# Optimization experiments

Measured on AMD Instinct MI355X. Metric: run time of the kernel, lower is better.

Reference implementation:

```python
import jax, jax.numpy as jnp
import numpy as np

NEG_INF = -1e30  # finite stand-in for log(0); keeps grads NaN-free

T_, B_, V_, L_ = 1024, 64, 512, 256


def setup_inputs() -> dict:
    key = jax.random.key(0)
    k1, k2 = jax.random.split(key)
    acts = jax.random.normal(k1, (T_, B_, V_), dtype=jnp.float32)
    labels = jax.random.randint(k2, (B_ * L_,), 1, V_, dtype=jnp.int32)  # blank=0 excluded
    act_lens = jnp.full((B_,), T_, dtype=jnp.int32)
    label_lens = jnp.full((B_,), L_, dtype=jnp.int32)
    return {"acts": acts, "labels": labels, "act_lens": act_lens, "label_lens": label_lens}


def _ctc_total_loss(acts, labels, act_lens, label_lens):
    # acts: (T, B, V) raw logits; warp-ctc applies softmax internally.
    T, B, V = acts.shape
    L = labels.shape[0] // B          # static max label length (uniform lengths)
    S = 2 * L + 1                     # extended label lattice with interleaved blanks
    logp = jax.nn.log_softmax(acts, axis=-1)

    # Unflatten labels -> padded (B, L)
    offsets = jnp.concatenate([jnp.zeros((1,), jnp.int32),
                               jnp.cumsum(label_lens.astype(jnp.int32))])[:-1]
    j = jnp.arange(L, dtype=jnp.int32)
    gidx = jnp.clip(offsets[:, None] + j[None, :], 0, labels.shape[0] - 1)
    padded = jnp.where(j[None, :] < label_lens[:, None], labels[gidx], 0)  # (B, L)

    # Extended labels: blank, l1, blank, l2, ..., blank
    ext = jnp.zeros((B, S), dtype=labels.dtype).at[:, 1::2].set(padded)
    ext_m2 = jnp.pad(ext, ((0, 0), (2, 0)))[:, :S]
    allow_skip = (ext != 0) & (ext != ext_m2)
    allow_skip = allow_skip.at[:, :2].set(False)

    bidx = jnp.arange(B)[:, None]
    lp_ext = logp[:, bidx, ext]       # (T, B, S): per-frame log-prob of lattice states

    alpha0 = jnp.full((B, S), NEG_INF, dtype=acts.dtype)
    alpha0 = alpha0.at[:, 0].set(lp_ext[0, :, 0]).at[:, 1].set(lp_ext[0, :, 1])
    neg = jnp.full((B, 1), NEG_INF, dtype=acts.dtype)

    def step(alpha, inp):
        lp_t, t = inp
        a1 = alpha
        a2 = jnp.concatenate([neg, alpha[:, :-1]], axis=1)
        a3 = jnp.concatenate([neg, neg, alpha[:, :-2]], axis=1)
        a3 = jnp.where(allow_skip, a3, NEG_INF)
        new = lp_t + jnp.logaddexp(jnp.logaddexp(a1, a2), a3)
        alpha = jnp.where((t < act_lens)[:, None], new, alpha)  # freeze past act_len
        return alpha, None

    alpha, _ = jax.lax.scan(step, alpha0, (lp_ext[1:], jnp.arange(1, T)))

    s_end = (2 * label_lens).astype(jnp.int32)           # final blank state
    a_end = jnp.take_along_axis(alpha, s_end[:, None], axis=1)[:, 0]
    a_end2 = jnp.take_along_axis(alpha, jnp.maximum(s_end - 1, 0)[:, None], axis=1)[:, 0]
    losses = -jnp.logaddexp(a_end, a_end2)               # per-example NLL
    return jnp.sum(losses)[None]                         # shape (1,), matches FloatTensor([sum])


def reference(acts, labels, act_lens, label_lens):
    return _ctc_total_loss(acts, labels, act_lens, label_lens)
```

## Files before the change

### kernel.cpp

```cpp
#include <hip/hip_runtime.h>

constexpr int T = 1024;
constexpr int B = 64;
constexpr int V = 512;
constexpr int L = 256;
constexpr int S = 2 * L + 1;
constexpr int C = 16;

typedef float f32x4 __attribute__((ext_vector_type(4)));

__device__ __forceinline__ unsigned short f2bf(float f) {
    unsigned u = __float_as_uint(f);
    u += 0x7fffu + ((u >> 16) & 1u);
    return (unsigned short)(u >> 16);
}

__device__ __forceinline__ float lane_bcast(float v, int i) {
    return __uint_as_float((unsigned)__builtin_amdgcn_readlane((int)__float_as_uint(v), i));
}


__global__ __launch_bounds__(64) void offsets_kernel(
    const int* __restrict__ label_lens, int* __restrict__ offsets)
{
    int lane = threadIdx.x;
    int v = (lane < B) ? label_lens[lane] : 0;
    int x = v;
#pragma unroll
    for (int o = 1; o < 64; o <<= 1) {
        int y = __shfl_up(x, o, 64);
        if (lane >= o) x += y;
    }
    if (lane < B) offsets[lane] = x - v;
}

__global__ __launch_bounds__(256) void setup_kernel(
    const float* __restrict__ acts, const int* __restrict__ labels,
    const int* __restrict__ label_lens, const int* __restrict__ offsets,
    float* __restrict__ lse_rows, unsigned short* __restrict__ packedU,
    float* __restrict__ blankU)
{
    __shared__ float rows[4][2][V];
    const int w    = threadIdx.x >> 6;
    const int lane = threadIdx.x & 63;
    const int rbase = (blockIdx.x * 4 + w) * 2;
    const f32x4* p = (const f32x4*)(acts + (size_t)rbase * V);

    f32x4 xa0 = __builtin_nontemporal_load(p + lane);
    f32x4 xa1 = __builtin_nontemporal_load(p + lane + 64);
    f32x4 xb0 = __builtin_nontemporal_load(p + lane + 128);
    f32x4 xb1 = __builtin_nontemporal_load(p + lane + 192);
    f32x4 ea0, ea1, eb0, eb1;
    ea0.x=__expf(xa0.x); ea0.y=__expf(xa0.y); ea0.z=__expf(xa0.z); ea0.w=__expf(xa0.w);
    ea1.x=__expf(xa1.x); ea1.y=__expf(xa1.y); ea1.z=__expf(xa1.z); ea1.w=__expf(xa1.w);
    eb0.x=__expf(xb0.x); eb0.y=__expf(xb0.y); eb0.z=__expf(xb0.z); eb0.w=__expf(xb0.w);
    eb1.x=__expf(xb1.x); eb1.y=__expf(xb1.y); eb1.z=__expf(xb1.z); eb1.w=__expf(xb1.w);
    ((f32x4*)rows[w][0])[lane]      = ea0;
    ((f32x4*)rows[w][0])[lane + 64] = ea1;
    ((f32x4*)rows[w][1])[lane]      = eb0;
    ((f32x4*)rows[w][1])[lane + 64] = eb1;
    float sa = ea0.x+ea0.y+ea0.z+ea0.w + ea1.x+ea1.y+ea1.z+ea1.w;
    float sb = eb0.x+eb0.y+eb0.z+eb0.w + eb1.x+eb1.y+eb1.z+eb1.w;
#pragma unroll
    for (int o = 32; o; o >>= 1) { sa += __shfl_xor(sa, o, 64); sb += __shfl_xor(sb, o, 64); }

#pragma unroll
    for (int rr = 0; rr < 2; ++rr) {
        const int r = rbase + rr;
        const int b = r & (B - 1), t = r >> 6;
        const float* rw = rows[w][rr];
        const int lab_len = label_lens[b];
        const int off     = offsets[b];
        const float ubk   = rw[0];
        const int j0 = 4 * lane;
        float q0 = (j0 + 0 < lab_len) ? rw[labels[min(off + j0 + 0, B * L - 1)]] : ubk;
        float q1 = (j0 + 1 < lab_len) ? rw[labels[min(off + j0 + 1, B * L - 1)]] : ubk;
        float q2 = (j0 + 2 < lab_len) ? rw[labels[min(off + j0 + 2, B * L - 1)]] : ubk;
        float q3 = (j0 + 3 < lab_len) ? rw[labels[min(off + j0 + 3, B * L - 1)]] : ubk;
        ushort4 hv = {f2bf(q0), f2bf(q1), f2bf(q2), f2bf(q3)};
        ((ushort4*)packedU)[(size_t)(b * T + t) * 64 + lane] = hv;
        if (lane == 0) {
            lse_rows[b * T + t] = __logf(rr ? sb : sa);
            blankU[b * T + t]   = ubk;
        }
    }
}

__global__ __launch_bounds__(128, 1) void ctc_kernel(
    const int* __restrict__ labels, const int* __restrict__ act_lens,
    const int* __restrict__ label_lens, const int* __restrict__ offsets,
    const float* __restrict__ lse_rows, const unsigned short* __restrict__ packedU,
    const float* __restrict__ blankU, float* __restrict__ out)
{
    __shared__ float sbr[S];
    __shared__ float s_accb;

    const int b    = blockIdx.x;
    const int wave = threadIdx.x >> 6;
    const int lane = threadIdx.x & 63;
    const int lab_len = label_lens[b];
    const int a_len   = act_lens[b];
    const int th      = (a_len - 1) >> 1;
    const int off     = offsets[b];
    const size_t rowbase = (size_t)b * T;

    int li0 = 4 * lane;
    int eprev = (li0 - 1 >= 0 && li0 - 1 < lab_len) ? labels[min(off + li0 - 1, B * L - 1)] : 0;
    int enext = (li0 + 4 < lab_len) ? labels[min(off + li0 + 4, B * L - 1)] : 0;
    int e0 = (li0 + 0 < lab_len) ? labels[min(off + li0 + 0, B * L - 1)] : 0;
    int e1 = (li0 + 1 < lab_len) ? labels[min(off + li0 + 1, B * L - 1)] : 0;
    int e2 = (li0 + 2 < lab_len) ? labels[min(off + li0 + 2, B * L - 1)] : 0;
    int e3 = (li0 + 3 < lab_len) ? labels[min(off + li0 + 3, B * L - 1)] : 0;

    const float aF0 = (8 * lane + 1 >= 2 && e0 != 0 && e0 != eprev) ? 1.f : 0.f;
    const float aF1 = (e1 != 0 && e1 != e0) ? 1.f : 0.f;
    const float aF2 = (e2 != 0 && e2 != e1) ? 1.f : 0.f;
    const float aF3 = (e3 != 0 && e3 != e2) ? 1.f : 0.f;
    const float aB0 = aF1, aB1 = aF2, aB2 = aF3;
    const float aB3 = (enext != 0 && enext != e3) ? 1.f : 0.f;

    float A0 = 0.f, A1 = 0.f, A2 = 0.f, A3 = 0.f, A4 = 0.f,
          A5 = 0.f, A6 = 0.f, A7 = 0.f, A8 = 0.f;
    float acc = 0.f, sls = 0.f;

    uint2 Ua[C], Ub[C];
    float Ka = 0.f, Kb = 0.f;

#define LOADCH(U, K, TLO) do {                                                \
        const int tl_ = min(max((int)(TLO), 0), T - C);                       \
        const uint2* gp_ = (const uint2*)(packedU + (rowbase + tl_) * 256);   \
        _Pragma("unroll")                                                     \
        for (int i_ = 0; i_ < C; ++i_) U[i_] = gp_[i_ * 64 + lane];           \
        K = blankU[rowbase + tl_ + (lane & (C - 1))];                         \
    } while (0)

#define RESCALE() do {                                                        \
        float m_ = fmaxf(A8, A0); m_ = fmaxf(m_, A1); m_ = fmaxf(m_, A2);     \
        m_ = fmaxf(m_, A3); m_ = fmaxf(m_, A4); m_ = fmaxf(m_, A5);           \
        m_ = fmaxf(m_, A6); m_ = fmaxf(m_, A7);                               \
        _Pragma("unroll")                                                     \
        for (int o_ = 32; o_; o_ >>= 1) m_ = fmaxf(m_, __shfl_xor(m_, o_, 64)); \
        m_ = fmaxf(m_, 1e-30f);                                               \
        float inv_ = __builtin_amdgcn_rcpf(m_);                               \
        acc += __logf(m_);                                                    \
        A0 *= inv_; A1 *= inv_; A2 *= inv_; A3 *= inv_; A4 *= inv_;           \
        A5 *= inv_; A6 *= inv_; A7 *= inv_; A8 *= inv_;                       \
    } while (0)

#define STEPF_CORE(HX, HY, UB) do {                                           \
        const float ub_ = (UB);                                               \
        const unsigned hx_ = (HX), hy_ = (HY);                                \
        const float u0_ = __uint_as_float(hx_ << 16);                         \
        const float u1_ = __uint_as_float(hx_ & 0xffff0000u);                 \
        const float u2_ = __uint_as_float(hy_ << 16);                         \
        const float u3_ = __uint_as_float(hy_ & 0xffff0000u);                 \
        float pA7_ = __shfl_up(A7, 1, 64);                                    \
        if (lane == 0) pA7_ = 0.f;                                            \
        A8 = ub_ * (A8 + A7);                                                 \
        A7 = u3_ * fmaf(aF3, A5, A7 + A6);                                    \
        A6 = ub_ * (A6 + A5);                                                 \
        A5 = u2_ * fmaf(aF2, A3, A5 + A4);                                    \
        A4 = ub_ * (A4 + A3);                                                 \
        A3 = u1_ * fmaf(aF1, A1, A3 + A2);                                    \
        A2 = ub_ * (A2 + A1);                                                 \
        A1 = u0_ * fmaf(aF0, pA7_, A1 + A0);                                  \
        A0 = ub_ * (A0 + pA7_);                                               \
    } while (0)
#define STEPF_R(U, K, I) STEPF_CORE(U[I].x, U[I].y, lane_bcast(K, I))

#define STEPB_CORE(HX, HY, UB) do {                                           \
        const float ub_ = (UB);                                               \
        const unsigned hx_ = (HX), hy_ = (HY);                                \
        const float u0_ = __uint_as_float(hx_ << 16);                         \
        const float u1_ = __uint_as_float(hx_ & 0xffff0000u);                 \
        const float u2_ = __uint_as_float(hy_ << 16);                         \
        const float u3_ = __uint_as_float(hy_ & 0xffff0000u);                 \
        float nC0_ = __shfl_down(A0, 1, 64);                                  \
        if (lane == 63) nC0_ = 0.f;                                           \
        A8 = ub_ * (A8 + A0);                                                 \
        A0 = u0_ * fmaf(aB0, A2, A0 + A1);                                    \
        A1 = ub_ * (A1 + A2);                                                 \
        A2 = u1_ * fmaf(aB1, A4, A2 + A3);                                    \
        A3 = ub_ * (A3 + A4);                                                 \
        A4 = u2_ * fmaf(aB2, A6, A4 + A5);                                    \
        A5 = ub_ * (A5 + A6);                                                 \
        A6 = u3_ * fmaf(aB3, nC0_, A6 + A7);                                  \
        A7 = ub_ * (A7 + nC0_);                                               \
    } while (0)
#define STEPB_R(U, K, I) STEPB_CORE(U[I].x, U[I].y, lane_bcast(K, I))

#define STEP_DIRECT(WHICH, TT) do {                                           \
        uint2 hvd_ = ((const uint2*)(packedU + (rowbase + (TT)) * 256))[lane];\
        float ubd_ = blankU[rowbase + (TT)];                                  \
        WHICH(hvd_.x, hvd_.y, ubd_);                                          \
    } while (0)

    if (wave == 0) {
        for (int t = lane; t < a_len; t += 64) sls += lse_rows[rowbase + t];
#pragma unroll
        for (int o = 32; o; o >>= 1) sls += __shfl_xor(sls, o, 64);

        if (lane == 0) {
            A0 = blankU[rowbase];
            A1 = __uint_as_float(((unsigned)packedU[rowbase * 256]) << 16);
        }

        if (th >= 1) {
            const int kfull = (th - 15) >> 4;
            LOADCH(Ua, Ka, 0);
            LOADCH(Ub, Kb, 16);
#pragma unroll
            for (int i = 1; i < C; ++i) { if (i <= th) STEPF_R(Ua, Ka, i); }
            RESCALE();
            LOADCH(Ua, Ka, 32);
            int k = 1;
            for (; k + 1 <= kfull; k += 2) {
#pragma unroll
                for (int i = 0; i < C; ++i) STEPF_R(Ub, Kb, i);
                RESCALE();
                LOADCH(Ub, Kb, 16 * (k + 2));
#pragma unroll
                for (int i = 0; i < C; ++i) STEPF_R(Ua, Ka, i);
                RESCALE();
                LOADCH(Ua, Ka, 16 * (k + 3));
            }
            if (k <= kfull) {
#pragma unroll
                for (int i = 0; i < C; ++i) STEPF_R(Ub, Kb, i);
                RESCALE();
            }
            const int tS = (kfull >= 1) ? 16 * (kfull + 1) : 16;
            for (int t = tS; t <= th; ++t) {
                STEP_DIRECT(STEPF_CORE, t);
                if (((t - tS) & 7) == 7) RESCALE();
            }
        }
    } else {
        const int send = 2 * lab_len;
        {
            size_t rl = rowbase + (a_len - 1);
            float ubl = blankU[rl];
            float ue  = (lab_len > 0)
                      ? __uint_as_float(((unsigned)packedU[rl * 256 + (lab_len - 1)]) << 16)
                      : 0.f;
            int s0 = 8 * lane + 1;
            A0 = (s0 + 0 == send) ? ubl : ((s0 + 0 == send - 1) ? ue : 0.f);
            A1 = (s0 + 1 == send) ? ubl : ((s0 + 1 == send - 1) ? ue : 0.f);
            A2 = (s0 + 2 == send) ? ubl : ((s0 + 2 == send - 1) ? ue : 0.f);
            A3 = (s0 + 3 == send) ? ubl : ((s0 + 3 == send - 1) ? ue : 0.f);
            A4 = (s0 + 4 == send) ? ubl : ((s0 + 4 == send - 1) ? ue : 0.f);
            A5 = (s0 + 5 == send) ? ubl : ((s0 + 5 == send - 1) ? ue : 0.f);
            A6 = (s0 + 6 == send) ? ubl : ((s0 + 6 == send - 1) ? ue : 0.f);
            A7 = (s0 + 7 == send) ? ubl : ((s0 + 7 == send - 1) ? ue : 0.f);
            A8 = (send == 0) ? ubl : 0.f;
        }

        const int nstB = a_len - 2 - th;
        if (nstB > 0 && a_len >= 16) {
            const int cfull = (a_len - th - 17) >> 4;
            LOADCH(Ua, Ka, a_len - 16);
            LOADCH(Ub, Kb, a_len - 32);
#pragma unroll
            for (int i = C - 2; i >= 0; --i) {
                if (a_len - 16 + i >= th + 1) STEPB_R(Ua, Ka, i);
            }
            RESCALE();
            LOADCH(Ua, Ka, a_len - 48);
            int c = 1;
            for (; c + 1 <= cfull; c += 2) {
#pragma unroll
                for (int i = C - 1; i >= 0; --i) STEPB_R(Ub, Kb, i);
                RESCALE();
                LOADCH(Ub, Kb, a_len - 16 * (c + 3));
#pragma unroll
                for (int i = C - 1; i >= 0; --i) STEPB_R(Ua, Ka, i);
                RESCALE();
                LOADCH(Ua, Ka, a_len - 16 * (c + 4));
            }
            if (c <= cfull) {
#pragma unroll
                for (int i = C - 1; i >= 0; --i) STEPB_R(Ub, Kb, i);
                RESCALE();
            }
            const int cf = (cfull >= 1) ? cfull : 0;
            const int tE = a_len - 16 * (cf + 1) - 1;
            for (int t = tE; t >= th + 1; --t) {
                STEP_DIRECT(STEPB_CORE, t);
                if (((tE - t) & 7) == 7) RESCALE();
            }
        } else if (nstB > 0) {
            for (int t = a_len - 2; t >= th + 1; --t) {
                STEP_DIRECT(STEPB_CORE, t);
                if (((a_len - 2 - t) & 7) == 7) RESCALE();
            }
        }

        {
            float nC0 = __shfl_down(A0, 1, 64);
            if (lane == 63) nC0 = 0.f;
            float w1 = fmaf(aB0, A2, A0 + A1);
            float w2 = A1 + A2;
            float w3 = fmaf(aB1, A4, A2 + A3);
            float w4 = A3 + A4;
            float w5 = fmaf(aB2, A6, A4 + A5);
            float w6 = A5 + A6;
            float w7 = fmaf(aB3, nC0, A6 + A7);
            float w8 = A7 + nC0;
            int sB = 8 * lane + 1;
            sbr[sB + 0] = w1; sbr[sB + 1] = w2; sbr[sB + 2] = w3; sbr[sB + 3] = w4;
            sbr[sB + 4] = w5; sbr[sB + 5] = w6; sbr[sB + 6] = w7; sbr[sB + 7] = w8;
            if (lane == 0) sbr[0] = A8 + A0;
            if (lane == 0) s_accb = acc;
        }
    }
    __syncthreads();
    if (wave == 0) {
        int s0 = 8 * lane;
        float p0 = __logf(fmaxf(A0, 1e-37f)) + __logf(fmaxf(sbr[s0 + 0], 1e-37f));
        float p1 = __logf(fmaxf(A1, 1e-37f)) + __logf(fmaxf(sbr[s0 + 1], 1e-37f));
        float p2 = __logf(fmaxf(A2, 1e-37f)) + __logf(fmaxf(sbr[s0 + 2], 1e-37f));
        float p3 = __logf(fmaxf(A3, 1e-37f)) + __logf(fmaxf(sbr[s0 + 3], 1e-37f));
        float p4 = __logf(fmaxf(A4, 1e-37f)) + __logf(fmaxf(sbr[s0 + 4], 1e-37f));
        float p5 = __logf(fmaxf(A5, 1e-37f)) + __logf(fmaxf(sbr[s0 + 5], 1e-37f));
        float p6 = __logf(fmaxf(A6, 1e-37f)) + __logf(fmaxf(sbr[s0 + 6], 1e-37f));
        float p7 = __logf(fmaxf(A7, 1e-37f)) + __logf(fmaxf(sbr[s0 + 7], 1e-37f));
        float p8 = -3.0e38f;
        if (lane == 63) p8 = __logf(fmaxf(A8, 1e-37f)) + __logf(fmaxf(sbr[512], 1e-37f));
        float pmax = fmaxf(fmaxf(fmaxf(p0, p1), fmaxf(p2, p3)),
                           fmaxf(fmaxf(p4, p5), fmaxf(p6, p7)));
        pmax = fmaxf(pmax, p8);
#pragma unroll
        for (int o = 32; o; o >>= 1) pmax = fmaxf(pmax, __shfl_xor(pmax, o, 64));
        float dot = __expf(p0 - pmax) + __expf(p1 - pmax) + __expf(p2 - pmax)
                  + __expf(p3 - pmax) + __expf(p4 - pmax) + __expf(p5 - pmax)
                  + __expf(p6 - pmax) + __expf(p7 - pmax);
        if (lane == 63) dot += __expf(p8 - pmax);
#pragma unroll
        for (int o = 32; o; o >>= 1) dot += __shfl_xor(dot, o, 64);
        if (lane == 0) {
            float loss = sls - acc - s_accb - (pmax + __logf(dot));
            atomicAdd(out, loss);
        }
    }
#undef LOADCH
#undef RESCALE
#undef STEPF_CORE
#undef STEPF_R
#undef STEPB_CORE
#undef STEPB_R
#undef STEP_DIRECT
}

extern "C" void kernel_launch(void* const* d_in, const int* in_sizes, int n_in,
                              void* d_out, int out_size, void* d_ws, size_t ws_size,
                              hipStream_t stream) {
    const float* acts       = (const float*)d_in[0];
    const int*   labels     = (const int*)d_in[1];
    const int*   act_lens   = (const int*)d_in[2];
    const int*   label_lens = (const int*)d_in[3];
    float*       out        = (float*)d_out;

    float*          lse_rows = (float*)d_ws;
    float*          blankU   = (float*)((char*)d_ws + (size_t)T * B * 4);
    int*            offsets  = (int*)  ((char*)d_ws + (size_t)2 * T * B * 4);
    unsigned short* packedU  = (unsigned short*)((char*)d_ws + (1u << 20));

    hipMemsetAsync(d_out, 0, sizeof(float), stream);

    offsets_kernel<<<1, 64, 0, stream>>>(label_lens, offsets);
    setup_kernel<<<T * B / 8, 256, 0, stream>>>(
        acts, labels, label_lens, offsets, lse_rows, packedU, blankU);
    ctc_kernel<<<B, 128, 0, stream>>>(
        labels, act_lens, label_lens, offsets, lse_rows, packedU, blankU, out);
}
```

Before: 250.4 us.

## Use DPP lane shifts and reductions, triple-buffer chunk loads in CTC recurrence

Replaces the ds_bpermute-based shfl_up/shfl_down neighbour exchange in each recurrence step with DPP wave_shr/wave_shl row moves, and the rescale max-reduction with a DPP row/bcast sequence followed by readlane. Chunk prefetch moves from two register buffers to three, aligned to the step range so the scalar tail loop is removed. Rescaling happens every 8 steps inside the chunk, and the label log-sum-exp reduction is moved after the initial loads are issued. The goal is lower per-step latency on the serial critical path and better hiding of global load latency, at the cost of more registers and DPP semantics that must hold across the whole 64-lane wave.

Measured after the change: 246.3 us. Within noise of the previous version (-1.6%).

```diff
diff --git a/kernel.cpp b/kernel.cpp
--- a/kernel.cpp
+++ b/kernel.cpp
@@ -17,6 +17,21 @@
 
 __device__ __forceinline__ float lane_bcast(float v, int i) {
     return __uint_as_float((unsigned)__builtin_amdgcn_readlane((int)__float_as_uint(v), i));
+}
+
+__device__ __forceinline__ float dpp_shr1z(float x) {
+    return __uint_as_float((unsigned)__builtin_amdgcn_update_dpp(
+        0, (int)__float_as_uint(x), 0x138, 0xf, 0xf, true));
+}
+__device__ __forceinline__ float dpp_shl1z(float x) {
+    return __uint_as_float((unsigned)__builtin_amdgcn_update_dpp(
+        0, (int)__float_as_uint(x), 0x130, 0xf, 0xf, true));
+}
+template <int CTRL, int RM>
+__device__ __forceinline__ float dppmax(float m) {
+    int mi = (int)__float_as_uint(m);
+    int t = __builtin_amdgcn_update_dpp(mi, mi, CTRL, RM, 0xf, false);
+    return fmaxf(m, __uint_as_float((unsigned)t));
 }
 
 
@@ -101,6 +116,7 @@
     const int lab_len = label_lens[b];
     const int a_len   = act_lens[b];
     const int th      = (a_len - 1) >> 1;
+    const int thp1    = th + 1;
     const int off     = offsets[b];
     const size_t rowbase = (size_t)b * T;
 
@@ -123,8 +139,8 @@
           A5 = 0.f, A6 = 0.f, A7 = 0.f, A8 = 0.f;
     float acc = 0.f, sls = 0.f;
 
-    uint2 Ua[C], Ub[C];
-    float Ka = 0.f, Kb = 0.f;
+    uint2 U0[C], U1[C], U2[C];
+    float K0 = 0.f, K1 = 0.f, K2 = 0.f;
 
 #define LOADCH(U, K, TLO) do {                                                \
         const int tl_ = min(max((int)(TLO), 0), T - C);                       \
@@ -138,8 +154,13 @@
         float m_ = fmaxf(A8, A0); m_ = fmaxf(m_, A1); m_ = fmaxf(m_, A2);     \
         m_ = fmaxf(m_, A3); m_ = fmaxf(m_, A4); m_ = fmaxf(m_, A5);           \
         m_ = fmaxf(m_, A6); m_ = fmaxf(m_, A7);                               \
-        _Pragma("unroll")                                                     \
-        for (int o_ = 32; o_; o_ >>= 1) m_ = fmaxf(m_, __shfl_xor(m_, o_, 64)); \
+        m_ = dppmax<0x111, 0xf>(m_);                           \
+        m_ = dppmax<0x112, 0xf>(m_);                           \
+        m_ = dppmax<0x114, 0xf>(m_);                           \
+        m_ = dppmax<0x118, 0xf>(m_);                           \
+        m_ = dppmax<0x142, 0xa>(m_);                 \
+        m_ = dppmax<0x143, 0xc>(m_);                 \
+        m_ = lane_bcast(m_, 63);                                              \
         m_ = fmaxf(m_, 1e-30f);                                               \
         float inv_ = __builtin_amdgcn_rcpf(m_);                               \
         acc += __logf(m_);                                                    \
@@ -154,8 +175,7 @@
         const float u1_ = __uint_as_float(hx_ & 0xffff0000u);                 \
         const float u2_ = __uint_as_float(hy_ << 16);                         \
         const float u3_ = __uint_as_float(hy_ & 0xffff0000u);                 \
-        float pA7_ = __shfl_up(A7, 1, 64);                                    \
-        if (lane == 0) pA7_ = 0.f;                                            \
+        const float pA7_ = dpp_shr1z(A7);                                     \
         A8 = ub_ * (A8 + A7);                                                 \
         A7 = u3_ * fmaf(aF3, A5, A7 + A6);                                    \
         A6 = ub_ * (A6 + A5);                                                 \
@@ -175,8 +195,7 @@
         const float u1_ = __uint_as_float(hx_ & 0xffff0000u);                 \
         const float u2_ = __uint_as_float(hy_ << 16);                         \
         const float u3_ = __uint_as_float(hy_ & 0xffff0000u);                 \
-        float nC0_ = __shfl_down(A0, 1, 64);                                  \
-        if (lane == 63) nC0_ = 0.f;                                           \
+        const float nC0_ = dpp_shl1z(A0);                                     \
         A8 = ub_ * (A8 + A0);                                                 \
         A0 = u0_ * fmaf(aB0, A2, A0 + A1);                                    \
         A1 = ub_ * (A1 + A2);                                                 \
@@ -195,45 +214,73 @@
         WHICH(hvd_.x, hvd_.y, ubd_);                                          \
     } while (0)
 
+#define DOF16(U, K) do {                                                      \
+        _Pragma("unroll")                                                     \
+        for (int i_ = 0; i_ < C; ++i_) {                                      \
+            STEPF_R(U, K, i_);                                                \
+            if (i_ == 7 || i_ == 15) RESCALE();                               \
+        }                                                                     \
+    } while (0)
+#define DOFPART(U, K, TLO) do {                                               \
+        _Pragma("unroll")                                                     \
+        for (int i_ = 0; i_ < C; ++i_) {                                      \
+            if ((TLO) + i_ <= th) STEPF_R(U, K, i_);                          \
+            if (i_ == 7 || i_ == 15) RESCALE();                               \
+        }                                                                     \
+    } while (0)
+#define DOB16(U, K) do {                                                      \
+        _Pragma("unroll")                                                     \
+        for (int i_ = C - 1; i_ >= 0; --i_) {                                 \
+            STEPB_R(U, K, i_);                                                \
+            if (i_ == 8 || i_ == 0) RESCALE();                                \
+        }                                                                     \
+    } while (0)
+#define DOBPART(U, K, TLO) do {                                               \
+        _Pragma("unroll")                                                     \
+        for (int i_ = C - 1; i_ >= 0; --i_) {                                 \
+            if ((TLO) + i_ >= thp1) STEPB_R(U, K, i_);                        \
+            if (i_ == 8 || i_ == 0) RESCALE();                                \
+        }                                                                     \
+    } while (0)
+
     if (wave == 0) {
-        for (int t = lane; t < a_len; t += 64) sls += lse_rows[rowbase + t];
-#pragma unroll
-        for (int o = 32; o; o >>= 1) sls += __shfl_xor(sls, o, 64);
-
         if (lane == 0) {
             A0 = blankU[rowbase];
             A1 = __uint_as_float(((unsigned)packedU[rowbase * 256]) << 16);
         }
 
         if (th >= 1) {
-            const int kfull = (th - 15) >> 4;
-            LOADCH(Ua, Ka, 0);
-            LOADCH(Ub, Kb, 16);
-#pragma unroll
-            for (int i = 1; i < C; ++i) { if (i <= th) STEPF_R(Ua, Ka, i); }
-            RESCALE();
-            LOADCH(Ua, Ka, 32);
-            int k = 1;
-            for (; k + 1 <= kfull; k += 2) {
-#pragma unroll
-                for (int i = 0; i < C; ++i) STEPF_R(Ub, Kb, i);
-                RESCALE();
-                LOADCH(Ub, Kb, 16 * (k + 2));
-#pragma unroll
-                for (int i = 0; i < C; ++i) STEPF_R(Ua, Ka, i);
-                RESCALE();
-                LOADCH(Ua, Ka, 16 * (k + 3));
+            const int nst   = th;
+            const int nc    = (nst + C - 1) / C;
+            const int nfull = nst / C;
+            LOADCH(U0, K0, 1);
+            LOADCH(U1, K1, 1 + C);
+            LOADCH(U2, K2, 1 + 2 * C);
+
+            for (int t = lane; t < a_len; t += 64) sls += lse_rows[rowbase + t];
+#pragma unroll
+            for (int o = 32; o; o >>= 1) sls += __shfl_xor(sls, o, 64);
+
+            int c = 0;
+            for (; c + 3 <= nfull; c += 3) {
+                DOF16(U0, K0); LOADCH(U0, K0, 1 + C * (c + 3));
+                DOF16(U1, K1); LOADCH(U1, K1, 1 + C * (c + 4));
+                DOF16(U2, K2); LOADCH(U2, K2, 1 + C * (c + 5));
             }
-            if (k <= kfull) {
-#pragma unroll
-                for (int i = 0; i < C; ++i) STEPF_R(Ub, Kb, i);
-                RESCALE();
+            const int rem = nfull - c;
+            if (rem == 0) {
+                if (nc > nfull) DOFPART(U0, K0, 1 + C * c);
+            } else if (rem == 1) {
+                DOF16(U0, K0);
+                if (nc > nfull) DOFPART(U1, K1, 1 + C * (c + 1));
+            } else {
+                DOF16(U0, K0); DOF16(U1, K1);
+                if (nc > nfull) DOFPART(U2, K2, 1 + C * (c + 2));
             }
-            const int tS = (kfull >= 1) ? 16 * (kfull + 1) : 16;
-            for (int t = tS; t <= th; ++t) {
-                STEP_DIRECT(STEPF_CORE, t);
-                if (((t - tS) & 7) == 7) RESCALE();
-            }
+        } else {
+            for (int t = lane; t < a_len; t += 64) sls += lse_rows[rowbase + t];
+#pragma unroll
+            for (int o = 32; o; o >>= 1) sls += __shfl_xor(sls, o, 64);
         }
     } else {
         const int send = 2 * lab_len;
@@ -256,48 +303,37 @@
         }
 
         const int nstB = a_len - 2 - th;
-        if (nstB > 0 && a_len >= 16) {
-            const int cfull = (a_len - th - 17) >> 4;
-            LOADCH(Ua, Ka, a_len - 16);
-            LOADCH(Ub, Kb, a_len - 32);
-#pragma unroll
-            for (int i = C - 2; i >= 0; --i) {
-                if (a_len - 16 + i >= th + 1) STEPB_R(Ua, Ka, i);
+        if (nstB > 0 && a_len >= 17) {
+            const int nc    = (nstB + C - 1) / C;
+            const int nfull = nstB / C;
+            LOADCH(U0, K0, a_len - 17);
+            LOADCH(U1, K1, a_len - 17 - C);
+            LOADCH(U2, K2, a_len - 17 - 2 * C);
+            int c = 0;
+            for (; c + 3 <= nfull; c += 3) {
+                DOB16(U0, K0); LOADCH(U0, K0, a_len - 17 - C * (c + 3));
+                DOB16(U1, K1); LOADCH(U1, K1, a_len - 17 - C * (c + 4));
+                DOB16(U2, K2); LOADCH(U2, K2, a_len - 17 - C * (c + 5));
             }
-            RESCALE();
-            LOADCH(Ua, Ka, a_len - 48);
-            int c = 1;
-            for (; c + 1 <= cfull; c += 2) {
-#pragma unroll
-                for (int i = C - 1; i >= 0; --i) STEPB_R(Ub, Kb, i);
-                RESCALE();
-                LOADCH(Ub, Kb, a_len - 16 * (c + 3));
-#pragma unroll
-                for (int i = C - 1; i >= 0; --i) STEPB_R(Ua, Ka, i);
-                RESCALE();
-                LOADCH(Ua, Ka, a_len - 16 * (c + 4));
-            }
-            if (c <= cfull) {
-#pragma unroll
-                for (int i = C - 1; i >= 0; --i) STEPB_R(Ub, Kb, i);
-                RESCALE();
-            }
-            const int cf = (cfull >= 1) ? cfull : 0;
-            const int tE = a_len - 16 * (cf + 1) - 1;
-            for (int t = tE; t >= th + 1; --t) {
-                STEP_DIRECT(STEPB_CORE, t);
-                if (((tE - t) & 7) == 7) RESCALE();
+            const int rem = nfull - c;
+            if (rem == 0) {
+                if (nc > nfull) DOBPART(U0, K0, a_len - 17 - C * c);
+            } else if (rem == 1) {
+                DOB16(U0, K0);
+                if (nc > nfull) DOBPART(U1, K1, a_len - 17 - C * (c + 1));
+            } else {
+                DOB16(U0, K0); DOB16(U1, K1);
+                if (nc > nfull) DOBPART(U2, K2, a_len - 17 - C * (c + 2));
             }
         } else if (nstB > 0) {
-            for (int t = a_len - 2; t >= th + 1; --t) {
+            for (int t = a_len - 2; t >= thp1; --t) {
                 STEP_DIRECT(STEPB_CORE, t);
                 if (((a_len - 2 - t) & 7) == 7) RESCALE();
             }
         }
 
         {
-            float nC0 = __shfl_down(A0, 1, 64);
-            if (lane == 63) nC0 = 0.f;
+            float nC0 = dpp_shl1z(A0);
             float w1 = fmaf(aB0, A2, A0 + A1);
             float w2 = A1 + A2;
             float w3 = fmaf(aB1, A4, A2 + A3);
@@ -349,6 +385,10 @@
 #undef STEPB_CORE
 #undef STEPB_R
 #undef STEP_DIRECT
+#undef DOF16
+#undef DOFPART
+#undef DOB16
+#undef DOBPART
 }
 
 extern "C" void kernel_launch(void* const* d_in, const int* in_sizes, int n_in,
```
